# Performance work log

Measured on AMD Instinct MI355X. Metric: run time of the kernel, lower is better.

The kernel has to match this reference:

```python
import jax, jax.numpy as jnp
import numpy as np

C = 64
INTER = C // 2  # 32
B, L = 4, 4096


def setup_inputs() -> dict:
    key = jax.random.key(0)
    ks = jax.random.split(key, 9)
    s_in = 1.0 / np.sqrt(C)
    s_inter = 1.0 / np.sqrt(INTER)
    return {
        "x": jax.random.normal(ks[0], (B, C, L), dtype=jnp.float32),
        "g_w": jax.random.normal(ks[1], (INTER, C), dtype=jnp.float32) * s_in,
        "g_b": jax.random.normal(ks[2], (INTER,), dtype=jnp.float32) * s_in,
        "theta_w": jax.random.normal(ks[3], (INTER, C), dtype=jnp.float32) * s_in,
        "theta_b": jax.random.normal(ks[4], (INTER,), dtype=jnp.float32) * s_in,
        "phi_w": jax.random.normal(ks[5], (INTER, C), dtype=jnp.float32) * s_in,
        "phi_b": jax.random.normal(ks[6], (INTER,), dtype=jnp.float32) * s_in,
        # NOTE: original inits W to zero (residual starts as identity); we use small
        # random values so the reference exercises the full computation.
        "W_w": jax.random.normal(ks[7], (C, INTER), dtype=jnp.float32) * s_inter,
        "W_b": jax.random.normal(ks[8], (C,), dtype=jnp.float32) * s_inter,
    }


def reference(x, g_w, g_b, theta_w, theta_b, phi_w, phi_b, W_w, W_b):
    # 1x1 Conv1d == channel matmul: [O,C] x [B,C,L] -> [B,O,L]
    g_x = jnp.einsum('oc,bcl->bol', g_w, x) + g_b[None, :, None]
    theta_x = jnp.einsum('oc,bcl->bol', theta_w, x) + theta_b[None, :, None]
    phi_x = jnp.einsum('oc,bcl->bol', phi_w, x) + phi_b[None, :, None]
    # f[b,l,m] = theta[:,l] . phi[:,m]  (unscaled attention scores, [B,L,L])
    f = jnp.einsum('bol,bom->blm', theta_x, phi_x)
    f_div_C = jax.nn.softmax(f, axis=-1)
    # y[b,o,l] = sum_m f[b,l,m] * g[b,o,m]
    y = jnp.einsum('blm,bom->bol', f_div_C, g_x)
    W_y = jnp.einsum('co,bol->bcl', W_w, y) + W_b[None, :, None]
    return W_y + x
```

## Files before the change

### kernel.cpp

```cpp
#include <hip/hip_runtime.h>

#define Bn 4
#define Cdim 64
#define INTER 32
#define Ln 4096
#define LOG2E 1.44269504088896340736f

typedef _Float16 half_t;
typedef __attribute__((ext_vector_type(8))) _Float16 half8v;
typedef __attribute__((ext_vector_type(4))) short short4v;
typedef __attribute__((ext_vector_type(8))) short short8v;
typedef __attribute__((ext_vector_type(4))) float f32x4;

__device__ __forceinline__ unsigned short f2bf(float f) {
    unsigned u = __float_as_uint(f);
    u += 0x7fffu + ((u >> 16) & 1u);
    return (unsigned short)(u >> 16);
}
__device__ __forceinline__ unsigned pack_bf(float a, float b) {
    unsigned ua = __float_as_uint(a) + 0x8000u;
    unsigned ub = __float_as_uint(b) + 0x8000u;
    return __builtin_amdgcn_perm(ub, ua, 0x07060302);
}
__device__ __forceinline__ void gll16(const void* g, void* l) {
    __builtin_amdgcn_global_load_lds(
        (const __attribute__((address_space(1))) unsigned int*)g,
        (__attribute__((address_space(3))) unsigned int*)l, 16, 0, 0);
}
__device__ __forceinline__ half8v cvt8(const float* p, float scale) {
    float4 f0 = *(const float4*)p;
    float4 f1 = *(const float4*)(p + 4);
    half_t h[8];
    h[0] = (half_t)(f0.x * scale); h[1] = (half_t)(f0.y * scale);
    h[2] = (half_t)(f0.z * scale); h[3] = (half_t)(f0.w * scale);
    h[4] = (half_t)(f1.x * scale); h[5] = (half_t)(f1.y * scale);
    h[6] = (half_t)(f1.z * scale); h[7] = (half_t)(f1.w * scale);
    half8v r;
    __builtin_memcpy(&r, h, 16);
    return r;
}

__global__ __launch_bounds__(192) void proj_kernel(
        const float* __restrict__ x,
        const float* __restrict__ g_w, const float* __restrict__ g_b,
        const float* __restrict__ th_w, const float* __restrict__ th_b,
        const float* __restrict__ ph_w, const float* __restrict__ ph_b,
        half_t* __restrict__ thfrag, half_t* __restrict__ phfrag,
        unsigned short* __restrict__ gfrag) {
    __shared__ half_t sx[64][72];
    __shared__ unsigned short sg[2048];
    int tid = threadIdx.x;
    int b = blockIdx.x >> 6;
    int l0 = (blockIdx.x & 63) << 6;

    for (int i = tid; i < 1024; i += 192) {
        int c = i >> 4, lq = (i & 15) << 2;
        float4 v = *(const float4*)&x[(size_t)(b * 64 + c) * Ln + l0 + lq];
        sx[lq + 0][c] = (half_t)v.x;
        sx[lq + 1][c] = (half_t)v.y;
        sx[lq + 2][c] = (half_t)v.z;
        sx[lq + 3][c] = (half_t)v.w;
    }
    __syncthreads();

    int lane = tid & 63, grp = tid >> 6;
    int l15 = lane & 15, quad = lane >> 4;

    const float* Wsrc = (grp == 0) ? th_w : (grp == 1) ? ph_w : g_w;
    const float* bsrc = (grp == 0) ? th_b : (grp == 1) ? ph_b : g_b;
    float scale = (grp == 0) ? LOG2E : 1.0f;

    half8v wA[2][2];
#pragma unroll
    for (int mf = 0; mf < 2; mf++)
#pragma unroll
        for (int kk = 0; kk < 2; kk++)
            wA[mf][kk] = cvt8(&Wsrc[(mf * 16 + l15) * 64 + kk * 32 + quad * 8], scale);
    half8v xB[4][2];
#pragma unroll
    for (int nf = 0; nf < 4; nf++)
#pragma unroll
        for (int kk = 0; kk < 2; kk++)
            xB[nf][kk] = *(const half8v*)&sx[nf * 16 + l15][kk * 32 + quad * 8];

    f32x4 acc[2][4];
    const f32x4 z = {0.f, 0.f, 0.f, 0.f};
#pragma unroll
    for (int mf = 0; mf < 2; mf++)
#pragma unroll
        for (int nf = 0; nf < 4; nf++) {
            f32x4 a = __builtin_amdgcn_mfma_f32_16x16x32_f16(wA[mf][0], xB[nf][0], z, 0, 0, 0);
            acc[mf][nf] = __builtin_amdgcn_mfma_f32_16x16x32_f16(wA[mf][1], xB[nf][1], a, 0, 0, 0);
        }
#pragma unroll
    for (int mf = 0; mf < 2; mf++) {
        float4 bv = *(const float4*)&bsrc[mf * 16 + quad * 4];
        float s0 = bv.x * scale, s1 = bv.y * scale, s2 = bv.z * scale, s3 = bv.w * scale;
#pragma unroll
        for (int nf = 0; nf < 4; nf++) {
            acc[mf][nf][0] += s0; acc[mf][nf][1] += s1;
            acc[mf][nf][2] += s2; acc[mf][nf][3] += s3;
        }
    }

    if (grp < 2) {
        half_t* F = (grp == 0) ? thfrag : phfrag;
#pragma unroll
        for (int mf = 0; mf < 2; mf++)
#pragma unroll
            for (int nf = 0; nf < 4; nf++) {
                half_t h[4];
                h[0] = (half_t)acc[mf][nf][0]; h[1] = (half_t)acc[mf][nf][1];
                h[2] = (half_t)acc[mf][nf][2]; h[3] = (half_t)acc[mf][nf][3];
                uint2 v;
                __builtin_memcpy(&v, h, 8);
                size_t u = (size_t)(b * 256 + (l0 >> 4) + nf) * 64 +
                           l15 + 16 * (mf * 2 + (quad >> 1));
                *(uint2*)(F + u * 8 + (quad & 1) * 4) = v;
            }
    } else {
#pragma unroll
        for (int mf = 0; mf < 2; mf++)
#pragma unroll
            for (int nf = 0; nf < 4; nf++)
#pragma unroll
                for (int r = 0; r < 4; r++) {
                    int lu = nf * 64 + (quad * 4 + r) + 16 * (l15 >> 2);
                    sg[lu * 8 + mf * 4 + (l15 & 3)] = f2bf(acc[mf][nf][r]);
                }
        __builtin_amdgcn_s_waitcnt(0);
        size_t base = (size_t)(b * 256 + (l0 >> 4)) * 512;
#pragma unroll
        for (int s = 0; s < 4; s++) {
            int i = lane + s * 64;
            uint4 v = ((const uint4*)sg)[i];
            *(uint4*)(gfrag + base + (size_t)i * 8) = v;
        }
    }
}

__global__ __launch_bounds__(256, 8) void attn_kernel(
        const half_t* __restrict__ thfrag, const half_t* __restrict__ phfrag,
        const unsigned short* __restrict__ gfrag,
        unsigned short* __restrict__ part, float* __restrict__ Sden,
        int KC, int CH) {
    __shared__ uint4 sbuf[2][512];

    int tid = threadIdx.x, lane = tid & 63, widx = tid >> 6;
    int l15 = lane & 15, quad = lane >> 4;

    int blk = blockIdx.x;
    int b = blk / (64 * KC);
    int rem = blk % (64 * KC);
    int qblk = rem / KC, kc = rem % KC;
    int qbase = qblk * 64 + widx * 16;
    int k0 = kc * CH;

    half8v th = *(const half8v*)(thfrag +
                                 ((size_t)(b * 256 + qblk * 4 + widx) * 64 + lane) * 8);

    unsigned short oh = (l15 == 0) ? 0x3F80 : 0;
    short4v ones;
    ones[0] = (short)oh; ones[1] = (short)oh; ones[2] = (short)oh; ones[3] = (short)oh;

    f32x4 acc0 = {0.f, 0.f, 0.f, 0.f};
    f32x4 acc1 = {0.f, 0.f, 0.f, 0.f};
    f32x4 accd = {0.f, 0.f, 0.f, 0.f};

    const char* phsrc = (const char*)(phfrag + (size_t)b * 256 * 512);
    const char* gsrc  = (const char*)(gfrag + (size_t)b * 256 * 512);
    const f32x4 z = {0.f, 0.f, 0.f, 0.f};

    gll16(phsrc + (size_t)(k0 >> 4) * 1024 + tid * 16, (char*)&sbuf[0][0] + tid * 16);
    gll16(gsrc + (size_t)(k0 >> 4) * 1024 + tid * 16, (char*)&sbuf[0][256] + tid * 16);
    __syncthreads();

    int cb = 0;
    for (int kt = k0; kt < k0 + CH; kt += 64) {
        if (kt + 64 < k0 + CH) {
            gll16(phsrc + (size_t)((kt + 64) >> 4) * 1024 + tid * 16,
                  (char*)&sbuf[cb ^ 1][0] + tid * 16);
            gll16(gsrc + (size_t)((kt + 64) >> 4) * 1024 + tid * 16,
                  (char*)&sbuf[cb ^ 1][256] + tid * 16);
        }
        const half_t* sph = (const half_t*)&sbuf[cb][0];
        const unsigned short* sg = (const unsigned short*)&sbuf[cb][256];
#pragma unroll
        for (int kf = 0; kf < 4; kf++) {
            half8v phA = *(const half8v*)(sph + kf * 512 + lane * 8);
            short8v g8 = *(const short8v*)(sg + kf * 512 + lane * 8);
            short4v ga0 = __builtin_shufflevector(g8, g8, 0, 1, 2, 3);
            short4v ga1 = __builtin_shufflevector(g8, g8, 4, 5, 6, 7);
            f32x4 s = __builtin_amdgcn_mfma_f32_16x16x32_f16(phA, th, z, 0, 0, 0);
            float p0 = __builtin_amdgcn_exp2f(s[0]);
            float p1 = __builtin_amdgcn_exp2f(s[1]);
            float p2 = __builtin_amdgcn_exp2f(s[2]);
            float p3 = __builtin_amdgcn_exp2f(s[3]);
            union { short4v s4; uint2 u2; } pb;
            pb.u2.x = pack_bf(p0, p1);
            pb.u2.y = pack_bf(p2, p3);
            acc0 = __builtin_amdgcn_mfma_f32_16x16x16bf16_1k(ga0, pb.s4, acc0, 0, 0, 0);
            acc1 = __builtin_amdgcn_mfma_f32_16x16x16bf16_1k(ga1, pb.s4, acc1, 0, 0, 0);
            accd = __builtin_amdgcn_mfma_f32_16x16x16bf16_1k(ones, pb.s4, accd, 0, 0, 0);
        }
        __syncthreads();
        cb ^= 1;
    }

    if (quad == 0) Sden[(size_t)(b * KC + kc) * Ln + qbase + l15] = accd[0];

    unsigned short* tbuf = (unsigned short*)&sbuf[0][0] + widx * 640;
    *(unsigned*)&tbuf[l15 * 40 + quad * 4]      = pack_bf(acc0[0], acc0[1]);
    *(unsigned*)&tbuf[l15 * 40 + quad * 4 + 2]  = pack_bf(acc0[2], acc0[3]);
    *(unsigned*)&tbuf[l15 * 40 + 16 + quad * 4]     = pack_bf(acc1[0], acc1[1]);
    *(unsigned*)&tbuf[l15 * 40 + 16 + quad * 4 + 2] = pack_bf(acc1[2], acc1[3]);
    __syncthreads();
    {
        int ql = lane >> 2, cq = (lane & 3) * 8;
        uint4 v = *(const uint4*)&tbuf[ql * 40 + cq];
        *(uint4*)(part + ((size_t)(b * KC + kc) * Ln + qbase + ql) * 32 + cq) = v;
    }
}

__global__ __launch_bounds__(256) void merge_kernel(
        const unsigned short* __restrict__ part, const float* __restrict__ Sden,
        const float* __restrict__ W_w, const float* __restrict__ W_b,
        const float* __restrict__ x, float* __restrict__ out, int KC) {
    int tid = threadIdx.x, lane = tid & 63, widx = tid >> 6;
    int l15 = lane & 15, quad = lane >> 4;
    int b = blockIdx.x >> 6;
    int t16 = (blockIdx.x & 63) * 4 + widx;
    int l = (t16 << 4) + l15;

    float den = 0.f;
    for (int kc = 0; kc < KC; kc++) den += Sden[(size_t)(b * KC + kc) * Ln + l];
    float inv = 1.f / den;

    float num[8] = {0.f, 0.f, 0.f, 0.f, 0.f, 0.f, 0.f, 0.f};
    for (int kc = 0; kc < KC; kc++) {
        uint4 v = *(const uint4*)&part[((size_t)(b * KC + kc) * Ln + l) * 32 + quad * 8];
        unsigned vv[4] = {v.x, v.y, v.z, v.w};
#pragma unroll
        for (int t = 0; t < 4; t++) {
            num[2 * t]     += __uint_as_float(vv[t] << 16);
            num[2 * t + 1] += __uint_as_float(vv[t] & 0xffff0000u);
        }
    }
    half_t yh[8];
#pragma unroll
    for (int j = 0; j < 8; j++) yh[j] = (half_t)(num[j] * inv);
    half8v yB;
    __builtin_memcpy(&yB, yh, 16);

    const f32x4 z = {0.f, 0.f, 0.f, 0.f};
    f32x4 acc[4];
#pragma unroll
    for (int mf = 0; mf < 4; mf++) {
        half8v wA = cvt8(&W_w[(mf * 16 + l15) * 32 + quad * 8], 1.0f);
        acc[mf] = __builtin_amdgcn_mfma_f32_16x16x32_f16(wA, yB, z, 0, 0, 0);
    }
#pragma unroll
    for (int mf = 0; mf < 4; mf++) {
        float4 bv = *(const float4*)&W_b[mf * 16 + quad * 4];
#pragma unroll
        for (int r = 0; r < 4; r++) {
            int c = mf * 16 + quad * 4 + r;
            size_t idx = (size_t)(b * 64 + c) * Ln + l;
            float bb = (r == 0) ? bv.x : (r == 1) ? bv.y : (r == 2) ? bv.z : bv.w;
            out[idx] = acc[mf][r] + bb + x[idx];
        }
    }
}

extern "C" void kernel_launch(void* const* d_in, const int* in_sizes, int n_in,
                              void* d_out, int out_size, void* d_ws, size_t ws_size,
                              hipStream_t stream) {
    const float* x    = (const float*)d_in[0];
    const float* g_w  = (const float*)d_in[1];
    const float* g_b  = (const float*)d_in[2];
    const float* th_w = (const float*)d_in[3];
    const float* th_b = (const float*)d_in[4];
    const float* ph_w = (const float*)d_in[5];
    const float* ph_b = (const float*)d_in[6];
    const float* W_w  = (const float*)d_in[7];
    const float* W_b  = (const float*)d_in[8];
    float* out = (float*)d_out;

    char* w = (char*)d_ws;
    const size_t off_th   = 0;
    const size_t off_ph   = 1048576;
    const size_t off_g    = 2097152;
    const size_t off_Sden = 3145728;

    int KC = 16;
    size_t off_part = 0;
    while (true) {
        off_part = off_Sden + (size_t)KC * (Bn * Ln * 4);
        off_part = (off_part + 255) & ~(size_t)255;
        size_t need = off_part + (size_t)KC * ((size_t)Bn * Ln * 32 * 2);
        if (need <= ws_size || KC == 1) break;
        KC >>= 1;
    }

    half_t* thfrag = (half_t*)(w + off_th);
    half_t* phfrag = (half_t*)(w + off_ph);
    unsigned short* gfrag = (unsigned short*)(w + off_g);
    float* Sden    = (float*)(w + off_Sden);
    unsigned short* part = (unsigned short*)(w + off_part);

    int CH = Ln / KC;

    proj_kernel<<<Bn * 64, 192, 0, stream>>>(x, g_w, g_b, th_w, th_b, ph_w, ph_b,
                                             thfrag, phfrag, gfrag);
    attn_kernel<<<Bn * 64 * KC, 256, 0, stream>>>(thfrag, phfrag, gfrag, part, Sden,
                                                  KC, CH);
    merge_kernel<<<Bn * 64, 256, 0, stream>>>(part, Sden, W_w, W_b, x, out, KC);
}
```

Baseline: 106.2 us.

## Process two query tiles per wave in attention and shrink key split count

Each attention wave now handles two 16-row query fragments, so every phi/g fragment loaded into LDS is reused twice. The key-axis split drops from 16 to 4 chunks, which shrinks the partial-result traffic and the merge work but leaves fewer, longer blocks. The P conversion switches to truncating bf16 packing, the launch-bounds occupancy hint is lowered, and the projection kernel is widened to 256 threads so the x load loop unrolls evenly. The trade-off is less parallelism and more registers per wave.

```diff
diff --git a/kernel.cpp b/kernel.cpp
--- a/kernel.cpp
+++ b/kernel.cpp
@@ -21,6 +21,9 @@
     unsigned ua = __float_as_uint(a) + 0x8000u;
     unsigned ub = __float_as_uint(b) + 0x8000u;
     return __builtin_amdgcn_perm(ub, ua, 0x07060302);
+}
+__device__ __forceinline__ unsigned pack_bf_t(float a, float b) {
+    return __builtin_amdgcn_perm(__float_as_uint(b), __float_as_uint(a), 0x07060302);
 }
 __device__ __forceinline__ void gll16(const void* g, void* l) {
     __builtin_amdgcn_global_load_lds(
@@ -40,7 +43,7 @@
     return r;
 }
 
-__global__ __launch_bounds__(192) void proj_kernel(
+__global__ __launch_bounds__(256) void proj_kernel(
         const float* __restrict__ x,
         const float* __restrict__ g_w, const float* __restrict__ g_b,
         const float* __restrict__ th_w, const float* __restrict__ th_b,
@@ -53,7 +56,9 @@
     int b = blockIdx.x >> 6;
     int l0 = (blockIdx.x & 63) << 6;
 
-    for (int i = tid; i < 1024; i += 192) {
+#pragma unroll
+    for (int p = 0; p < 4; p++) {
+        int i = tid + p * 256;
         int c = i >> 4, lq = (i & 15) << 2;
         float4 v = *(const float4*)&x[(size_t)(b * 64 + c) * Ln + l0 + lq];
         sx[lq + 0][c] = (half_t)v.x;
@@ -64,6 +69,7 @@
     __syncthreads();
 
     int lane = tid & 63, grp = tid >> 6;
+    if (grp == 3) return;
     int l15 = lane & 15, quad = lane >> 4;
 
     const float* Wsrc = (grp == 0) ? th_w : (grp == 1) ? ph_w : g_w;
@@ -139,7 +145,7 @@
     }
 }
 
-__global__ __launch_bounds__(256, 8) void attn_kernel(
+__global__ __launch_bounds__(256, 2) void attn_kernel(
         const half_t* __restrict__ thfrag, const half_t* __restrict__ phfrag,
         const unsigned short* __restrict__ gfrag,
         unsigned short* __restrict__ part, float* __restrict__ Sden,
@@ -150,22 +156,29 @@
     int l15 = lane & 15, quad = lane >> 4;
 
     int blk = blockIdx.x;
-    int b = blk / (64 * KC);
-    int rem = blk % (64 * KC);
+    int b = blk / (32 * KC);
+    int rem = blk % (32 * KC);
     int qblk = rem / KC, kc = rem % KC;
-    int qbase = qblk * 64 + widx * 16;
+    int qbase = qblk * 128 + widx * 32;
     int k0 = kc * CH;
 
-    half8v th = *(const half8v*)(thfrag +
-                                 ((size_t)(b * 256 + qblk * 4 + widx) * 64 + lane) * 8);
+    half8v th[2];
+#pragma unroll
+    for (int qf = 0; qf < 2; qf++)
+        th[qf] = *(const half8v*)(thfrag +
+                                  ((size_t)(b * 256 + (qbase >> 4) + qf) * 64 + lane) * 8);
 
     unsigned short oh = (l15 == 0) ? 0x3F80 : 0;
     short4v ones;
     ones[0] = (short)oh; ones[1] = (short)oh; ones[2] = (short)oh; ones[3] = (short)oh;
 
-    f32x4 acc0 = {0.f, 0.f, 0.f, 0.f};
-    f32x4 acc1 = {0.f, 0.f, 0.f, 0.f};
-    f32x4 accd = {0.f, 0.f, 0.f, 0.f};
+    f32x4 acc[2][2], accd[2];
+#pragma unroll
+    for (int qf = 0; qf < 2; qf++) {
+        acc[qf][0] = (f32x4){0.f, 0.f, 0.f, 0.f};
+        acc[qf][1] = (f32x4){0.f, 0.f, 0.f, 0.f};
+        accd[qf]   = (f32x4){0.f, 0.f, 0.f, 0.f};
+    }
 
     const char* phsrc = (const char*)(phfrag + (size_t)b * 256 * 512);
     const char* gsrc  = (const char*)(gfrag + (size_t)b * 256 * 512);
@@ -191,34 +204,54 @@
             short8v g8 = *(const short8v*)(sg + kf * 512 + lane * 8);
             short4v ga0 = __builtin_shufflevector(g8, g8, 0, 1, 2, 3);
             short4v ga1 = __builtin_shufflevector(g8, g8, 4, 5, 6, 7);
-            f32x4 s = __builtin_amdgcn_mfma_f32_16x16x32_f16(phA, th, z, 0, 0, 0);
-            float p0 = __builtin_amdgcn_exp2f(s[0]);
-            float p1 = __builtin_amdgcn_exp2f(s[1]);
-            float p2 = __builtin_amdgcn_exp2f(s[2]);
-            float p3 = __builtin_amdgcn_exp2f(s[3]);
-            union { short4v s4; uint2 u2; } pb;
-            pb.u2.x = pack_bf(p0, p1);
-            pb.u2.y = pack_bf(p2, p3);
-            acc0 = __builtin_amdgcn_mfma_f32_16x16x16bf16_1k(ga0, pb.s4, acc0, 0, 0, 0);
-            acc1 = __builtin_amdgcn_mfma_f32_16x16x16bf16_1k(ga1, pb.s4, acc1, 0, 0, 0);
-            accd = __builtin_amdgcn_mfma_f32_16x16x16bf16_1k(ones, pb.s4, accd, 0, 0, 0);
+#pragma unroll
+            for (int qf = 0; qf < 2; qf++) {
+                f32x4 s = __builtin_amdgcn_mfma_f32_16x16x32_f16(phA, th[qf], z, 0, 0, 0);
+                float p0 = __builtin_amdgcn_exp2f(s[0]);
+                float p1 = __builtin_amdgcn_exp2f(s[1]);
+                float p2 = __builtin_amdgcn_exp2f(s[2]);
+                float p3 = __builtin_amdgcn_exp2f(s[3]);
+                union { short4v s4; uint2 u2; } pb;
+                pb.u2.x = pack_bf_t(p0, p1);
+                pb.u2.y = pack_bf_t(p2, p3);
+                acc[qf][0] = __builtin_amdgcn_mfma_f32_16x16x16bf16_1k(ga0, pb.s4,
+                                                                      acc[qf][0], 0, 0, 0);
+                acc[qf][1] = __builtin_amdgcn_mfma_f32_16x16x16bf16_1k(ga1, pb.s4,
+                                                                      acc[qf][1], 0, 0, 0);
+                accd[qf] = __builtin_amdgcn_mfma_f32_16x16x16bf16_1k(ones, pb.s4,
+                                                                    accd[qf], 0, 0, 0);
+            }
         }
         __syncthreads();
         cb ^= 1;
     }
 
-    if (quad == 0) Sden[(size_t)(b * KC + kc) * Ln + qbase + l15] = accd[0];
-
-    unsigned short* tbuf = (unsigned short*)&sbuf[0][0] + widx * 640;
-    *(unsigned*)&tbuf[l15 * 40 + quad * 4]      = pack_bf(acc0[0], acc0[1]);
-    *(unsigned*)&tbuf[l15 * 40 + quad * 4 + 2]  = pack_bf(acc0[2], acc0[3]);
-    *(unsigned*)&tbuf[l15 * 40 + 16 + quad * 4]     = pack_bf(acc1[0], acc1[1]);
-    *(unsigned*)&tbuf[l15 * 40 + 16 + quad * 4 + 2] = pack_bf(acc1[2], acc1[3]);
-    __syncthreads();
+    size_t sb = (size_t)(b * KC + kc) * Ln + qbase;
+    if (quad == 0) {
+        Sden[sb + l15] = accd[0][0];
+        Sden[sb + 16 + l15] = accd[1][0];
+    }
+
+    unsigned short* tb = (unsigned short*)&sbuf[0][0] + widx * 1280;
+#pragma unroll
+    for (int qf = 0; qf < 2; qf++) {
+        int qr = qf * 16 + l15;
+#pragma unroll
+        for (int cf = 0; cf < 2; cf++) {
+            uint2 v;
+            v.x = pack_bf(acc[qf][cf][0], acc[qf][cf][1]);
+            v.y = pack_bf(acc[qf][cf][2], acc[qf][cf][3]);
+            *(uint2*)&tb[qr * 40 + cf * 16 + quad * 4] = v;
+        }
+    }
+    __builtin_amdgcn_s_waitcnt(0);
     {
-        int ql = lane >> 2, cq = (lane & 3) * 8;
-        uint4 v = *(const uint4*)&tbuf[ql * 40 + cq];
-        *(uint4*)(part + ((size_t)(b * KC + kc) * Ln + qbase + ql) * 32 + cq) = v;
+        int r = lane >> 1, h = lane & 1;
+        uint4 v0 = *(const uint4*)&tb[r * 40 + h * 16];
+        uint4 v1 = *(const uint4*)&tb[r * 40 + h * 16 + 8];
+        unsigned short* dst = part + ((size_t)(b * KC + kc) * Ln + qbase + r) * 32 + h * 16;
+        *(uint4*)dst = v0;
+        *(uint4*)(dst + 8) = v1;
     }
 }
 
@@ -292,7 +325,7 @@
     const size_t off_g    = 2097152;
     const size_t off_Sden = 3145728;
 
-    int KC = 16;
+    int KC = 4;
     size_t off_part = 0;
     while (true) {
         off_part = off_Sden + (size_t)KC * (Bn * Ln * 4);
@@ -310,9 +343,9 @@
 
     int CH = Ln / KC;
 
-    proj_kernel<<<Bn * 64, 192, 0, stream>>>(x, g_w, g_b, th_w, th_b, ph_w, ph_b,
+    proj_kernel<<<Bn * 64, 256, 0, stream>>>(x, g_w, g_b, th_w, th_b, ph_w, ph_b,
                                              thfrag, phfrag, gfrag);
-    attn_kernel<<<Bn * 64 * KC, 256, 0, stream>>>(thfrag, phfrag, gfrag, part, Sden,
+    attn_kernel<<<Bn * 32 * KC, 256, 0, stream>>>(thfrag, phfrag, gfrag, part, Sden,
                                                   KC, CH);
     merge_kernel<<<Bn * 64, 256, 0, stream>>>(part, Sden, W_w, W_b, x, out, KC);
 }
```

Result: faster. 98.45 us (-7.3%).
